# Performance work log

Hardware: AMD Instinct MI355X
Metric: run time of the kernel (lower is better)

The kernel has to match this reference:

```python
import jax, jax.numpy as jnp
import numpy as np

ENC_DIM, DEC_DIM, ATT_DIM = 512, 512, 512
B, S = 32, 4096


def setup_inputs() -> dict:
    key = jax.random.key(0)
    ks = jax.random.split(key, 8)
    sc = lambda d: 1.0 / np.sqrt(d)
    return {
        "input": jax.random.normal(ks[0], (B, S, ENC_DIM), dtype=jnp.float32),
        "dec_h": jax.random.normal(ks[1], (B, DEC_DIM), dtype=jnp.float32),
        "W_enc": jax.random.uniform(ks[2], (ENC_DIM, ATT_DIM), jnp.float32, -sc(ENC_DIM), sc(ENC_DIM)),
        "b_enc": jax.random.uniform(ks[3], (ATT_DIM,), jnp.float32, -sc(ENC_DIM), sc(ENC_DIM)),
        "W_dec": jax.random.uniform(ks[4], (DEC_DIM, ATT_DIM), jnp.float32, -sc(DEC_DIM), sc(DEC_DIM)),
        "b_dec": jax.random.uniform(ks[5], (ATT_DIM,), jnp.float32, -sc(DEC_DIM), sc(DEC_DIM)),
        "w_att": jax.random.uniform(ks[6], (ATT_DIM, 1), jnp.float32, -sc(ATT_DIM), sc(ATT_DIM)),
        "b_att": jax.random.uniform(ks[7], (1,), jnp.float32, -sc(ATT_DIM), sc(ATT_DIM)),
    }


def reference(input, dec_h, W_enc, b_enc, W_dec, b_dec, w_att, b_att):
    # enc_att: [B,S,A]; dec_att: [B,A] broadcast over S
    enc_att = jnp.einsum("bse,ea->bsa", input, W_enc) + b_enc
    dec_att = dec_h @ W_dec + b_dec
    # score: [B,S]
    att = jax.nn.relu(enc_att + dec_att[:, None, :]) @ w_att + b_att  # [B,S,1]
    prob = jax.nn.softmax(att, axis=1)  # softmax over sequence dim
    weighted = jnp.sum(input * prob, axis=1)  # [B,enc_dim]
    return weighted, prob[..., 0]
```

## Files before the change

kernel.cpp:

```cpp
#include <hip/hip_runtime.h>
#include <hip/hip_bf16.h>

typedef __attribute__((ext_vector_type(4))) float f32x4;
typedef __attribute__((ext_vector_type(8))) __bf16 bf16x8;
typedef __attribute__((ext_vector_type(4))) unsigned int u32x4;


__device__ __forceinline__ float lo_bf(unsigned int u) {
  return __builtin_bit_cast(float, u << 16);
}
__device__ __forceinline__ float hi_bf(unsigned int u) {
  return __builtin_bit_cast(float, u & 0xffff0000u);
}

__global__ void prep_w(const float* __restrict__ W_enc, unsigned short* __restrict__ Wf) {
  int idx = blockIdx.x * 256 + threadIdx.x;
  int lane = idx & 63;
  int grp = idx >> 6;
  int ntile = grp >> 4, kb = grp & 15;
  int n = ntile * 16 + (lane & 15);
  int k0 = kb * 32 + (lane >> 4) * 8;
  unsigned short* dst = Wf + idx * 8;
  #pragma unroll
  for (int j = 0; j < 8; ++j) {
    float f = W_enc[(k0 + j) * 512 + n];
    dst[j] = __builtin_bit_cast(unsigned short, (__bf16)f);
  }
}

__global__ void prep_c(const float* __restrict__ dec_h, const float* __restrict__ W_dec,
                       const float* __restrict__ b_dec, const float* __restrict__ b_enc,
                       float* __restrict__ c_vec) {
  int idx = blockIdx.x * 256 + threadIdx.x;
  int b = idx >> 9, a = idx & 511;
  float s = b_dec[a] + b_enc[a];
  const float* dh = dec_h + b * 512;
  for (int k = 0; k < 512; ++k) s += dh[k] * W_dec[k * 512 + a];
  c_vec[idx] = s;
}

__global__ __launch_bounds__(512, 4) void attn_main(
    const float* __restrict__ input, const unsigned short* __restrict__ Wf,
    const float* __restrict__ c_vec, const float* __restrict__ w_att,
    float* __restrict__ att_out, float* __restrict__ m_out, float* __restrict__ pw_out) {
  __shared__ u32x4 A4[4096];
  __shared__ float c_lds[512];
  __shared__ float w_lds[512];
  __shared__ float red[8][64];
  __shared__ float p_lds[64];

  char* Al = (char*)A4;
  float* redf = &red[0][0];
  const int tid = threadIdx.x;
  const int wave = tid >> 6, lane = tid & 63;
  const int l15 = lane & 15, l4 = lane >> 4;
  const int blk = blockIdx.x;
  const int b = blk >> 6;
  const int chunk = blk & 63;

  if (tid < 512) {
    c_lds[tid] = c_vec[b * 512 + tid];
    w_lds[tid] = w_att[tid];
  }

  const float* Abase = input + (long)(b * 4096 + chunk * 64) * 512;
  float4 f[8][2];
  #pragma unroll
  for (int i = 0; i < 8; ++i) {
    int ch = tid + i * 512;
    int row = ch >> 6, c16 = ch & 63;
    const float4* src = (const float4*)(Abase + row * 512 + c16 * 8);
    f[i][0] = src[0];
    f[i][1] = src[1];
  }
  #pragma unroll
  for (int i = 0; i < 8; ++i) {
    int ch = tid + i * 512;
    int row = ch >> 6, c16 = ch & 63;
    bf16x8 v;
    v[0] = (__bf16)f[i][0].x; v[1] = (__bf16)f[i][0].y;
    v[2] = (__bf16)f[i][0].z; v[3] = (__bf16)f[i][0].w;
    v[4] = (__bf16)f[i][1].x; v[5] = (__bf16)f[i][1].y;
    v[6] = (__bf16)f[i][1].z; v[7] = (__bf16)f[i][1].w;
    int byte = row * 1024 + ((c16 * 16) ^ ((row & 7) << 4));
    *(bf16x8*)(Al + byte) = v;
  }
  __syncthreads();

  f32x4 acc[4][4];
  #pragma unroll
  for (int mi = 0; mi < 4; ++mi)
    #pragma unroll
    for (int nj = 0; nj < 4; ++nj) {
      f32x4 z = {0.f, 0.f, 0.f, 0.f};
      acc[mi][nj] = z;
    }

  const bf16x8* Wfp = (const bf16x8*)Wf;
  const int w4 = wave * 4;

  for (int kb = 0; kb < 16; ++kb) {
    bf16x8 bv[4];
    #pragma unroll
    for (int nj = 0; nj < 4; ++nj)
      bv[nj] = Wfp[((w4 + nj) * 16 + kb) * 64 + lane];
    bf16x8 afr[4];
    #pragma unroll
    for (int mi = 0; mi < 4; ++mi) {
      int row = mi * 16 + l15;
      int byte = row * 1024 + (((kb * 64) + l4 * 16) ^ ((row & 7) << 4));
      afr[mi] = *(const bf16x8*)(Al + byte);
    }
    #pragma unroll
    for (int nj = 0; nj < 4; ++nj)
      #pragma unroll
      for (int mi = 0; mi < 4; ++mi)
        acc[mi][nj] = __builtin_amdgcn_mfma_f32_16x16x32_bf16(afr[mi], bv[nj], acc[mi][nj], 0, 0, 0);
  }

  float attp[16];
  #pragma unroll
  for (int i = 0; i < 16; ++i) attp[i] = 0.f;
  #pragma unroll
  for (int nj = 0; nj < 4; ++nj) {
    int n = (w4 + nj) * 16 + l15;
    float cc = c_lds[n], ww = w_lds[n];
    #pragma unroll
    for (int mi = 0; mi < 4; ++mi)
      #pragma unroll
      for (int r = 0; r < 4; ++r)
        attp[mi * 4 + r] += fmaxf(acc[mi][nj][r] + cc, 0.f) * ww;
  }
  #pragma unroll
  for (int off = 1; off < 16; off <<= 1)
    #pragma unroll
    for (int i = 0; i < 16; ++i)
      attp[i] += __shfl_xor(attp[i], off, 64);
  if (l15 == 0) {
    #pragma unroll
    for (int mi = 0; mi < 4; ++mi)
      #pragma unroll
      for (int r = 0; r < 4; ++r)
        red[wave][mi * 16 + l4 * 4 + r] = attp[mi * 4 + r];
  }
  __syncthreads();

  if (tid < 64) {
    float av = red[0][tid] + red[1][tid] + red[2][tid] + red[3][tid]
             + red[4][tid] + red[5][tid] + red[6][tid] + red[7][tid];
    att_out[b * 4096 + chunk * 64 + tid] = av;
    float m = av;
    #pragma unroll
    for (int off = 32; off >= 1; off >>= 1) m = fmaxf(m, __shfl_xor(m, off, 64));
    p_lds[tid] = expf(av - m);
    if (tid == 0) m_out[blk] = m;
  }
  __syncthreads();

  const int c2 = (tid & 255) * 2;
  const int h = tid >> 8;
  float pw0 = 0.f, pw1 = 0.f;
  #pragma unroll 8
  for (int i = 0; i < 32; ++i) {
    int s = h * 32 + i;
    float p = p_lds[s];
    unsigned int u = *(const unsigned int*)(Al + s * 1024 + ((c2 * 2) ^ ((s & 7) << 4)));
    pw0 += p * lo_bf(u);
    pw1 += p * hi_bf(u);
  }
  if (h == 1) { redf[c2] = pw0; redf[c2 + 1] = pw1; }
  __syncthreads();
  if (h == 0) {
    pw_out[blk * 512 + c2]     = pw0 + redf[c2];
    pw_out[blk * 512 + c2 + 1] = pw1 + redf[c2 + 1];
  }
}

__global__ void finalize(const float* __restrict__ att, const float* __restrict__ m_blk,
                         const float* __restrict__ pw, float* __restrict__ out) {
  const int b = blockIdx.x, tid = threadIdx.x;
  const int wave = tid >> 6, lane = tid & 63;
  __shared__ float wred[4];
  __shared__ float zred[4];
  __shared__ float fac[64];

  float v[16];
  float mx = -3.4e38f;
  #pragma unroll
  for (int i = 0; i < 16; ++i) {
    v[i] = att[b * 4096 + i * 256 + tid];
    mx = fmaxf(mx, v[i]);
  }
  #pragma unroll
  for (int off = 32; off >= 1; off >>= 1) mx = fmaxf(mx, __shfl_xor(mx, off, 64));
  if (lane == 0) wred[wave] = mx;
  __syncthreads();
  mx = fmaxf(fmaxf(wred[0], wred[1]), fmaxf(wred[2], wred[3]));

  float z = 0.f;
  #pragma unroll
  for (int i = 0; i < 16; ++i) { v[i] = expf(v[i] - mx); z += v[i]; }
  #pragma unroll
  for (int off = 32; off >= 1; off >>= 1) z += __shfl_xor(z, off, 64);
  if (lane == 0) zred[wave] = z;
  __syncthreads();
  z = zred[0] + zred[1] + zred[2] + zred[3];
  float invZ = 1.f / z;

  #pragma unroll
  for (int i = 0; i < 16; ++i)
    out[16384 + b * 4096 + i * 256 + tid] = v[i] * invZ;

  if (tid < 64) fac[tid] = expf(m_blk[b * 64 + tid] - mx) * invZ;
  __syncthreads();

  int e = tid * 2;
  float w0 = 0.f, w1 = 0.f;
  for (int s = 0; s < 64; ++s) {
    float f = fac[s];
    const float* row = pw + (b * 64 + s) * 512;
    w0 += f * row[e];
    w1 += f * row[e + 1];
  }
  out[b * 512 + e] = w0;
  out[b * 512 + e + 1] = w1;
}

extern "C" void kernel_launch(void* const* d_in, const int* in_sizes, int n_in,
                              void* d_out, int out_size, void* d_ws, size_t ws_size,
                              hipStream_t stream) {
  const float* input = (const float*)d_in[0];
  const float* dec_h = (const float*)d_in[1];
  const float* W_enc = (const float*)d_in[2];
  const float* b_enc = (const float*)d_in[3];
  const float* W_dec = (const float*)d_in[4];
  const float* b_dec = (const float*)d_in[5];
  const float* w_att = (const float*)d_in[6];
  float* out = (float*)d_out;

  char* ws = (char*)d_ws;
  unsigned short* Wf = (unsigned short*)(ws);
  float* c_vec = (float*)(ws + 524288);
  float* att   = (float*)(ws + 589824);
  float* m_b   = (float*)(ws + 1114112);
  float* pw    = (float*)(ws + 1122304);

  hipLaunchKernelGGL(prep_w, dim3(128), dim3(256), 0, stream, W_enc, Wf);
  hipLaunchKernelGGL(prep_c, dim3(64), dim3(256), 0, stream, dec_h, W_dec, b_dec, b_enc, c_vec);
  hipLaunchKernelGGL(attn_main, dim3(2048), dim3(512), 0, stream, input, Wf, c_vec, w_att, att, m_b, pw);
  hipLaunchKernelGGL(finalize, dim3(32), dim3(256), 0, stream, att, m_b, pw, out);
}
```

Baseline: 125.0 us.

## Make attention kernel persistent over 8 chunks with prefetch, split prep and finalize

The main kernel now runs 256 blocks of 1024 threads. Each block loops over 8 consecutive 64-row chunks and prefetches the next chunk's fp32 input into registers while it computes the current one. The goal is to overlap global loads with MFMA work and to cut per-block setup cost. prep_c is split four ways along K into partial sums that attn_main adds together, and finalize is spread over 4x more blocks, both to expose more parallelism in the small kernels. The risks are more register pressure at 1024 threads and extra syncs per chunk, and the 256-block grid may leave some CUs underused.

```diff
diff --git a/kernel.cpp b/kernel.cpp
--- a/kernel.cpp
+++ b/kernel.cpp
@@ -5,13 +5,6 @@
 typedef __attribute__((ext_vector_type(8))) __bf16 bf16x8;
 typedef __attribute__((ext_vector_type(4))) unsigned int u32x4;
 
-
-__device__ __forceinline__ float lo_bf(unsigned int u) {
-  return __builtin_bit_cast(float, u << 16);
-}
-__device__ __forceinline__ float hi_bf(unsigned int u) {
-  return __builtin_bit_cast(float, u & 0xffff0000u);
-}
 
 __global__ void prep_w(const float* __restrict__ W_enc, unsigned short* __restrict__ Wf) {
   int idx = blockIdx.x * 256 + threadIdx.x;
@@ -30,155 +23,165 @@
 
 __global__ void prep_c(const float* __restrict__ dec_h, const float* __restrict__ W_dec,
                        const float* __restrict__ b_dec, const float* __restrict__ b_enc,
-                       float* __restrict__ c_vec) {
-  int idx = blockIdx.x * 256 + threadIdx.x;
-  int b = idx >> 9, a = idx & 511;
-  float s = b_dec[a] + b_enc[a];
-  const float* dh = dec_h + b * 512;
-  for (int k = 0; k < 512; ++k) s += dh[k] * W_dec[k * 512 + a];
-  c_vec[idx] = s;
-}
-
-__global__ __launch_bounds__(512, 4) void attn_main(
+                       float* __restrict__ cpart) {
+  int b = blockIdx.x >> 2, j = blockIdx.x & 3;
+  int a = threadIdx.x;
+  const float* dh = dec_h + b * 512 + j * 128;
+  const float* wd = W_dec + (j * 128) * 512 + a;
+  float s = (j == 0) ? (b_dec[a] + b_enc[a]) : 0.f;
+  #pragma unroll 8
+  for (int k = 0; k < 128; ++k) s += dh[k] * wd[k * 512];
+  cpart[j * 16384 + b * 512 + a] = s;
+}
+
+__global__ __launch_bounds__(1024, 4) void attn_main(
     const float* __restrict__ input, const unsigned short* __restrict__ Wf,
-    const float* __restrict__ c_vec, const float* __restrict__ w_att,
+    const float* __restrict__ cpart, const float* __restrict__ w_att,
     float* __restrict__ att_out, float* __restrict__ m_out, float* __restrict__ pw_out) {
   __shared__ u32x4 A4[4096];
   __shared__ float c_lds[512];
   __shared__ float w_lds[512];
-  __shared__ float red[8][64];
+  __shared__ float red[16][64];
   __shared__ float p_lds[64];
 
   char* Al = (char*)A4;
-  float* redf = &red[0][0];
   const int tid = threadIdx.x;
   const int wave = tid >> 6, lane = tid & 63;
   const int l15 = lane & 15, l4 = lane >> 4;
   const int blk = blockIdx.x;
-  const int b = blk >> 6;
-  const int chunk = blk & 63;
+  const int ci0 = blk * 8;
+  const int b = ci0 >> 6;
 
   if (tid < 512) {
-    c_lds[tid] = c_vec[b * 512 + tid];
+    c_lds[tid] = cpart[tid + b * 512] + cpart[16384 + tid + b * 512]
+               + cpart[32768 + tid + b * 512] + cpart[49152 + tid + b * 512];
     w_lds[tid] = w_att[tid];
   }
 
-  const float* Abase = input + (long)(b * 4096 + chunk * 64) * 512;
-  float4 f[8][2];
-  #pragma unroll
+  float4 fa[4][2];
+
+  auto LOADS = [&](int ci) {
+    const float* base = input + (long)ci * 32768;
+    #pragma unroll
+    for (int u = 0; u < 4; ++u) {
+      int ch = tid + u * 1024;
+      int row = ch >> 6, c32 = ch & 63;
+      const float4* s4 = (const float4*)(base + row * 512 + c32 * 8);
+      fa[u][0] = s4[0];
+      fa[u][1] = s4[1];
+    }
+  };
+  auto WRITECONV = [&]() {
+    #pragma unroll
+    for (int u = 0; u < 4; ++u) {
+      int ch = tid + u * 1024;
+      int row = ch >> 6, c32 = ch & 63;
+      bf16x8 v;
+      v[0] = (__bf16)fa[u][0].x; v[1] = (__bf16)fa[u][0].y;
+      v[2] = (__bf16)fa[u][0].z; v[3] = (__bf16)fa[u][0].w;
+      v[4] = (__bf16)fa[u][1].x; v[5] = (__bf16)fa[u][1].y;
+      v[6] = (__bf16)fa[u][1].z; v[7] = (__bf16)fa[u][1].w;
+      *(bf16x8*)(Al + row * 1024 + ((c32 * 16) ^ ((row & 7) << 4))) = v;
+    }
+  };
+
+  const bf16x8* Wfp = (const bf16x8*)Wf;
+  const int w2 = wave * 2;
+  const bf16x8* wbase = Wfp + (w2 * 16) * 64 + lane;
+
+  LOADS(ci0);
+  WRITECONV();
+  __syncthreads();
+
   for (int i = 0; i < 8; ++i) {
-    int ch = tid + i * 512;
-    int row = ch >> 6, c16 = ch & 63;
-    const float4* src = (const float4*)(Abase + row * 512 + c16 * 8);
-    f[i][0] = src[0];
-    f[i][1] = src[1];
-  }
-  #pragma unroll
-  for (int i = 0; i < 8; ++i) {
-    int ch = tid + i * 512;
-    int row = ch >> 6, c16 = ch & 63;
-    bf16x8 v;
-    v[0] = (__bf16)f[i][0].x; v[1] = (__bf16)f[i][0].y;
-    v[2] = (__bf16)f[i][0].z; v[3] = (__bf16)f[i][0].w;
-    v[4] = (__bf16)f[i][1].x; v[5] = (__bf16)f[i][1].y;
-    v[6] = (__bf16)f[i][1].z; v[7] = (__bf16)f[i][1].w;
-    int byte = row * 1024 + ((c16 * 16) ^ ((row & 7) << 4));
-    *(bf16x8*)(Al + byte) = v;
-  }
-  __syncthreads();
-
-  f32x4 acc[4][4];
-  #pragma unroll
-  for (int mi = 0; mi < 4; ++mi)
-    #pragma unroll
-    for (int nj = 0; nj < 4; ++nj) {
+    const int ci = ci0 + i;
+    if (i < 7) LOADS(ci + 1);
+
+    f32x4 acc[4][2];
+    #pragma unroll
+    for (int mi = 0; mi < 4; ++mi) {
       f32x4 z = {0.f, 0.f, 0.f, 0.f};
-      acc[mi][nj] = z;
-    }
-
-  const bf16x8* Wfp = (const bf16x8*)Wf;
-  const int w4 = wave * 4;
-
-  for (int kb = 0; kb < 16; ++kb) {
-    bf16x8 bv[4];
-    #pragma unroll
-    for (int nj = 0; nj < 4; ++nj)
-      bv[nj] = Wfp[((w4 + nj) * 16 + kb) * 64 + lane];
-    bf16x8 afr[4];
-    #pragma unroll
-    for (int mi = 0; mi < 4; ++mi) {
-      int row = mi * 16 + l15;
-      int byte = row * 1024 + (((kb * 64) + l4 * 16) ^ ((row & 7) << 4));
-      afr[mi] = *(const bf16x8*)(Al + byte);
-    }
-    #pragma unroll
-    for (int nj = 0; nj < 4; ++nj)
+      acc[mi][0] = z; acc[mi][1] = z;
+    }
+    #pragma unroll 4
+    for (int kb = 0; kb < 16; ++kb) {
+      bf16x8 bv0 = wbase[kb * 64];
+      bf16x8 bv1 = wbase[(16 + kb) * 64];
+      #pragma unroll
+      for (int mi = 0; mi < 4; ++mi) {
+        int row = mi * 16 + l15;
+        bf16x8 afr = *(const bf16x8*)(Al + row * 1024 + (((kb * 64) + l4 * 16) ^ ((row & 7) << 4)));
+        acc[mi][0] = __builtin_amdgcn_mfma_f32_16x16x32_bf16(afr, bv0, acc[mi][0], 0, 0, 0);
+        acc[mi][1] = __builtin_amdgcn_mfma_f32_16x16x32_bf16(afr, bv1, acc[mi][1], 0, 0, 0);
+      }
+    }
+
+    float attp[16];
+    #pragma unroll
+    for (int q = 0; q < 16; ++q) attp[q] = 0.f;
+    #pragma unroll
+    for (int nj = 0; nj < 2; ++nj) {
+      int n = (w2 + nj) * 16 + l15;
+      float cc = c_lds[n], ww = w_lds[n];
       #pragma unroll
       for (int mi = 0; mi < 4; ++mi)
-        acc[mi][nj] = __builtin_amdgcn_mfma_f32_16x16x32_bf16(afr[mi], bv[nj], acc[mi][nj], 0, 0, 0);
-  }
-
-  float attp[16];
-  #pragma unroll
-  for (int i = 0; i < 16; ++i) attp[i] = 0.f;
-  #pragma unroll
-  for (int nj = 0; nj < 4; ++nj) {
-    int n = (w4 + nj) * 16 + l15;
-    float cc = c_lds[n], ww = w_lds[n];
-    #pragma unroll
-    for (int mi = 0; mi < 4; ++mi)
-      #pragma unroll
-      for (int r = 0; r < 4; ++r)
-        attp[mi * 4 + r] += fmaxf(acc[mi][nj][r] + cc, 0.f) * ww;
-  }
-  #pragma unroll
-  for (int off = 1; off < 16; off <<= 1)
-    #pragma unroll
-    for (int i = 0; i < 16; ++i)
-      attp[i] += __shfl_xor(attp[i], off, 64);
-  if (l15 == 0) {
-    #pragma unroll
-    for (int mi = 0; mi < 4; ++mi)
-      #pragma unroll
-      for (int r = 0; r < 4; ++r)
-        red[wave][mi * 16 + l4 * 4 + r] = attp[mi * 4 + r];
-  }
-  __syncthreads();
-
-  if (tid < 64) {
-    float av = red[0][tid] + red[1][tid] + red[2][tid] + red[3][tid]
-             + red[4][tid] + red[5][tid] + red[6][tid] + red[7][tid];
-    att_out[b * 4096 + chunk * 64 + tid] = av;
-    float m = av;
-    #pragma unroll
-    for (int off = 32; off >= 1; off >>= 1) m = fmaxf(m, __shfl_xor(m, off, 64));
-    p_lds[tid] = expf(av - m);
-    if (tid == 0) m_out[blk] = m;
-  }
-  __syncthreads();
-
-  const int c2 = (tid & 255) * 2;
-  const int h = tid >> 8;
-  float pw0 = 0.f, pw1 = 0.f;
-  #pragma unroll 8
-  for (int i = 0; i < 32; ++i) {
-    int s = h * 32 + i;
-    float p = p_lds[s];
-    unsigned int u = *(const unsigned int*)(Al + s * 1024 + ((c2 * 2) ^ ((s & 7) << 4)));
-    pw0 += p * lo_bf(u);
-    pw1 += p * hi_bf(u);
-  }
-  if (h == 1) { redf[c2] = pw0; redf[c2 + 1] = pw1; }
-  __syncthreads();
-  if (h == 0) {
-    pw_out[blk * 512 + c2]     = pw0 + redf[c2];
-    pw_out[blk * 512 + c2 + 1] = pw1 + redf[c2 + 1];
+        #pragma unroll
+        for (int r = 0; r < 4; ++r)
+          attp[mi * 4 + r] += fmaxf(acc[mi][nj][r] + cc, 0.f) * ww;
+    }
+    #pragma unroll
+    for (int off = 1; off < 16; off <<= 1)
+      #pragma unroll
+      for (int q = 0; q < 16; ++q)
+        attp[q] += __shfl_xor(attp[q], off, 64);
+    if (l15 == 0) {
+      #pragma unroll
+      for (int mi = 0; mi < 4; ++mi)
+        #pragma unroll
+        for (int r = 0; r < 4; ++r)
+          red[wave][mi * 16 + l4 * 4 + r] = attp[mi * 4 + r];
+    }
+    __syncthreads();
+
+    if (tid < 64) {
+      float av = 0.f;
+      #pragma unroll
+      for (int w = 0; w < 16; ++w) av += red[w][tid];
+      att_out[b * 4096 + (ci & 63) * 64 + tid] = av;
+      float m = av;
+      #pragma unroll
+      for (int off = 32; off >= 1; off >>= 1) m = fmaxf(m, __shfl_xor(m, off, 64));
+      p_lds[tid] = expf(av - m);
+      if (tid == 0) m_out[ci] = m;
+    }
+    __syncthreads();
+
+    {
+      int col = tid >> 1, h = tid & 1;
+      int ebyte = (col >> 1) * 4;
+      unsigned int sh = (col & 1) ? 0u : 16u;
+      float pwa = 0.f;
+      #pragma unroll 8
+      for (int s = h * 32; s < h * 32 + 32; ++s) {
+        float p = p_lds[s];
+        unsigned int u = *(const unsigned int*)(Al + s * 1024 + (ebyte ^ ((s & 7) << 4)));
+        pwa += p * __builtin_bit_cast(float, (u << sh) & 0xffff0000u);
+      }
+      pwa += __shfl_xor(pwa, 1, 64);
+      if (h == 0) pw_out[ci * 512 + col] = pwa;
+    }
+    __syncthreads();
+
+    if (i < 7) WRITECONV();
+    __syncthreads();
   }
 }
 
 __global__ void finalize(const float* __restrict__ att, const float* __restrict__ m_blk,
                          const float* __restrict__ pw, float* __restrict__ out) {
-  const int b = blockIdx.x, tid = threadIdx.x;
+  const int bg = blockIdx.x;
+  const int b = bg >> 2, g = bg & 3;
+  const int tid = threadIdx.x;
   const int wave = tid >> 6, lane = tid & 63;
   __shared__ float wred[4];
   __shared__ float zred[4];
@@ -208,22 +211,22 @@
   float invZ = 1.f / z;
 
   #pragma unroll
-  for (int i = 0; i < 16; ++i)
-    out[16384 + b * 4096 + i * 256 + tid] = v[i] * invZ;
+  for (int i = 0; i < 4; ++i) {
+    int ii = g * 4 + i;
+    out[16384 + b * 4096 + ii * 256 + tid] = v[ii] * invZ;
+  }
 
   if (tid < 64) fac[tid] = expf(m_blk[b * 64 + tid] - mx) * invZ;
   __syncthreads();
 
-  int e = tid * 2;
-  float w0 = 0.f, w1 = 0.f;
-  for (int s = 0; s < 64; ++s) {
-    float f = fac[s];
-    const float* row = pw + (b * 64 + s) * 512;
-    w0 += f * row[e];
-    w1 += f * row[e + 1];
-  }
-  out[b * 512 + e] = w0;
-  out[b * 512 + e + 1] = w1;
+  int col = g * 128 + (tid >> 1);
+  int h = tid & 1;
+  float w0 = 0.f;
+  #pragma unroll 8
+  for (int s = h * 32; s < h * 32 + 32; ++s)
+    w0 += fac[s] * pw[(b * 64 + s) * 512 + col];
+  w0 += __shfl_xor(w0, 1, 64);
+  if (h == 0) out[b * 512 + col] = w0;
 }
 
 extern "C" void kernel_launch(void* const* d_in, const int* in_sizes, int n_in,
@@ -240,13 +243,13 @@
 
   char* ws = (char*)d_ws;
   unsigned short* Wf = (unsigned short*)(ws);
-  float* c_vec = (float*)(ws + 524288);
-  float* att   = (float*)(ws + 589824);
-  float* m_b   = (float*)(ws + 1114112);
-  float* pw    = (float*)(ws + 1122304);
+  float* cpart = (float*)(ws + 524288);
+  float* att   = (float*)(ws + 786432);
+  float* m_b   = (float*)(ws + 1310720);
+  float* pw    = (float*)(ws + 1318912);
 
   hipLaunchKernelGGL(prep_w, dim3(128), dim3(256), 0, stream, W_enc, Wf);
-  hipLaunchKernelGGL(prep_c, dim3(64), dim3(256), 0, stream, dec_h, W_dec, b_dec, b_enc, c_vec);
-  hipLaunchKernelGGL(attn_main, dim3(2048), dim3(512), 0, stream, input, Wf, c_vec, w_att, att, m_b, pw);
-  hipLaunchKernelGGL(finalize, dim3(32), dim3(256), 0, stream, att, m_b, pw, out);
-}
+  hipLaunchKernelGGL(prep_c, dim3(128), dim3(512), 0, stream, dec_h, W_dec, b_dec, b_enc, cpart);
+  hipLaunchKernelGGL(attn_main, dim3(256), dim3(1024), 0, stream, input, Wf, cpart, w_att, att, m_b, pw);
+  hipLaunchKernelGGL(finalize, dim3(128), dim3(256), 0, stream, att, m_b, pw, out);
+}
```

Result: slower. 148.2 us (+18.6%).
